# Kernel optimization log

Measured on AMD Instinct MI355X. Metric: run time of the kernel, lower is better.

The kernel has to match this reference:

```python
import jax, jax.numpy as jnp
import numpy as np

N = 50000
HEADS = 8
NEG_SLOPE = 0.2


def gat_layer(x, W, a_src, a_dst, b, src, dst, heads, n):
    # x: [N, Fin], W: [Fin, heads*C], a_src/a_dst: [heads, C], b: [heads*C]
    C = W.shape[1] // heads
    h = (x @ W).reshape(n, heads, C)                      # [N, H, C]
    al_s = jnp.einsum('nhc,hc->nh', h, a_src)             # [N, H]
    al_d = jnp.einsum('nhc,hc->nh', h, a_dst)             # [N, H]
    e = al_s[src] + al_d[dst]                             # [E, H]
    e = jnp.where(e > 0, e, NEG_SLOPE * e)                # LeakyReLU(0.2)
    # segment softmax over incoming edges of each destination node
    emax = jax.ops.segment_max(e, dst, num_segments=n)
    ex = jnp.exp(e - emax[dst])
    denom = jax.ops.segment_sum(ex, dst, num_segments=n)
    alpha = ex / denom[dst]                               # [E, H]
    out = jax.ops.segment_sum(h[src] * alpha[:, :, None], dst, num_segments=n)
    return out.reshape(n, heads * C) + b


def setup_inputs() -> dict:
    key = jax.random.key(0)
    ks = jax.random.split(key, 32)
    d_in, d_h, d_out = 128, 128, 128
    C = d_h // HEADS
    E = 800000
    x = jax.random.normal(ks[0], (N, d_in), dtype=jnp.float32)
    edge_index = jax.random.randint(ks[1], (2, E), 0, N, dtype=jnp.int64)
    edge_attr = jax.random.normal(ks[2], (E, 16), dtype=jnp.float32)
    s = lambda fan: 1.0 / np.sqrt(fan)
    inp = {'x': x, 'edge_index': edge_index, 'edge_attr': edge_attr}
    ki = 3
    for i in range(1, 5):
        fin = d_in if i == 1 else d_h
        inp[f'W{i}'] = jax.random.normal(ks[ki], (fin, d_h), jnp.float32) * s(fin); ki += 1
        inp[f'a_src{i}'] = jax.random.normal(ks[ki], (HEADS, C), jnp.float32) * s(C); ki += 1
        inp[f'a_dst{i}'] = jax.random.normal(ks[ki], (HEADS, C), jnp.float32) * s(C); ki += 1
        inp[f'b{i}'] = jnp.zeros((d_h,), jnp.float32)
    # conv5: heads=1, out=hidden
    inp['W5'] = jax.random.normal(ks[ki], (d_h, d_h), jnp.float32) * s(d_h); ki += 1
    inp['a_src5'] = jax.random.normal(ks[ki], (1, d_h), jnp.float32) * s(d_h); ki += 1
    inp['a_dst5'] = jax.random.normal(ks[ki], (1, d_h), jnp.float32) * s(d_h); ki += 1
    inp['b5'] = jnp.zeros((d_h,), jnp.float32)
    inp['W_lin'] = jax.random.normal(ks[ki], (d_h, d_out), jnp.float32) * s(d_h); ki += 1
    inp['b_lin'] = jnp.zeros((d_out,), jnp.float32)
    return inp


def reference(x, edge_index, edge_attr,
              W1, a_src1, a_dst1, b1,
              W2, a_src2, a_dst2, b2,
              W3, a_src3, a_dst3, b3,
              W4, a_src4, a_dst4, b4,
              W5, a_src5, a_dst5, b5,
              W_lin, b_lin):
    n = x.shape[0]
    # PyG GATConv adds self loops by default
    ar = jnp.arange(n, dtype=edge_index.dtype)
    src = jnp.concatenate([edge_index[0], ar])
    dst = jnp.concatenate([edge_index[1], ar])
    h = jax.nn.relu(gat_layer(x, W1, a_src1, a_dst1, b1, src, dst, HEADS, n))
    h = jax.nn.relu(gat_layer(h, W2, a_src2, a_dst2, b2, src, dst, HEADS, n))
    h = jax.nn.relu(gat_layer(h, W3, a_src3, a_dst3, b3, src, dst, HEADS, n))
    h = jax.nn.relu(gat_layer(h, W4, a_src4, a_dst4, b4, src, dst, HEADS, n))
    h = jax.nn.relu(gat_layer(h, W5, a_src5, a_dst5, b5, src, dst, 1, n))
    return jax.nn.relu(h @ W_lin + b_lin)
```

## Files before the change

### kernel.cpp

```cpp
#include <hip/hip_runtime.h>


__global__ __launch_bounds__(256) void k_deg_init(int* deg, int n) {
  int i = blockIdx.x * 256 + threadIdx.x;
  if (i < n) deg[i] = 1;
}

__global__ __launch_bounds__(256) void k_count(const int* __restrict__ ei, int E, int* deg) {
  int i = blockIdx.x * 256 + threadIdx.x;
  if (i < E) atomicAdd(&deg[ei[E + i]], 1);
}

__device__ __forceinline__ int block_excl_scan(int v, int* tot) {
  __shared__ int wsum[4];
  int lane = threadIdx.x & 63, w = threadIdx.x >> 6;
  int x = v;
  #pragma unroll
  for (int off = 1; off < 64; off <<= 1) {
    int y = __shfl_up(x, off);
    if (lane >= off) x += y;
  }
  if (lane == 63) wsum[w] = x;
  __syncthreads();
  int wbase = 0;
  #pragma unroll
  for (int i = 0; i < 4; i++) wbase += (i < w) ? wsum[i] : 0;
  if (tot) *tot = wsum[0] + wsum[1] + wsum[2] + wsum[3];
  return wbase + x - v;
}

__global__ __launch_bounds__(256) void k_bsum(const int* __restrict__ deg, int* __restrict__ bsum, int n) {
  int i = blockIdx.x * 256 + threadIdx.x;
  int v = (i < n) ? deg[i] : 0;
  int tot;
  block_excl_scan(v, &tot);
  if (threadIdx.x == 0) bsum[blockIdx.x] = tot;
}

__global__ __launch_bounds__(256) void k_bscan(const int* __restrict__ bsum, int* __restrict__ boff, int nb) {
  int t = threadIdx.x;
  int v = (t < nb) ? bsum[t] : 0;
  int ex = block_excl_scan(v, nullptr);
  if (t < nb) boff[t] = ex;
}

__global__ __launch_bounds__(256) void k_rowptr(const int* __restrict__ deg,
                                                const int* __restrict__ boff,
                                                int* __restrict__ row_ptr,
                                                int* __restrict__ cursor, int n) {
  int i = blockIdx.x * 256 + threadIdx.x;
  int v = (i < n) ? deg[i] : 0;
  int ex = block_excl_scan(v, nullptr) + boff[blockIdx.x];
  if (i < n) { row_ptr[i] = ex; cursor[i] = ex; }
  if (i == n - 1) row_ptr[n] = ex + v;
}

__global__ __launch_bounds__(256) void k_fill(const int* __restrict__ ei, int E, int n,
                                              int* cursor, int* __restrict__ srcs) {
  int i = blockIdx.x * 256 + threadIdx.x;
  if (i >= E + n) return;
  int s, d;
  if (i < E) { s = ei[i]; d = ei[E + i]; }
  else       { s = i - E; d = s; }
  int slot = atomicAdd(&cursor[d], 1);
  srcs[slot] = s;
}

__global__ __launch_bounds__(256) void k_gemm(const float* __restrict__ A,
                                              const float* __restrict__ W,
                                              const float* __restrict__ bias,
                                              float* __restrict__ C, int M, int relu) {
  __shared__ float As[32][65];
  __shared__ float Bs[32][128];
  int tid = threadIdx.x;
  int row0 = blockIdx.x * 64;
  int tx = tid & 15;
  int ty = tid >> 4;
  float acc[4][8] = {};
  for (int kt = 0; kt < 128; kt += 32) {
    #pragma unroll
    for (int i = 0; i < 2; i++) {
      int idx = tid + i * 256;
      int r = idx >> 3;
      int k4 = (idx & 7) << 2;
      float4 v = make_float4(0.f, 0.f, 0.f, 0.f);
      int gr = row0 + r;
      if (gr < M) v = *(const float4*)(A + (size_t)gr * 128 + kt + k4);
      As[k4 + 0][r] = v.x; As[k4 + 1][r] = v.y; As[k4 + 2][r] = v.z; As[k4 + 3][r] = v.w;
    }
    #pragma unroll
    for (int i = 0; i < 4; i++) {
      int idx = tid + i * 256;
      int k = idx >> 5;
      int n4 = (idx & 31) << 2;
      *(float4*)(&Bs[k][n4]) = *(const float4*)(W + (size_t)(kt + k) * 128 + n4);
    }
    __syncthreads();
    #pragma unroll
    for (int k = 0; k < 32; k++) {
      float a0 = As[k][ty * 4 + 0], a1 = As[k][ty * 4 + 1];
      float a2 = As[k][ty * 4 + 2], a3 = As[k][ty * 4 + 3];
      float b[8];
      *(float4*)&b[0] = *(const float4*)&Bs[k][tx * 8];
      *(float4*)&b[4] = *(const float4*)&Bs[k][tx * 8 + 4];
      #pragma unroll
      for (int j = 0; j < 8; j++) {
        acc[0][j] += a0 * b[j];
        acc[1][j] += a1 * b[j];
        acc[2][j] += a2 * b[j];
        acc[3][j] += a3 * b[j];
      }
    }
    __syncthreads();
  }
  #pragma unroll
  for (int i = 0; i < 4; i++) {
    int r = row0 + ty * 4 + i;
    if (r >= M) continue;
    #pragma unroll
    for (int j4 = 0; j4 < 8; j4 += 4) {
      int c = tx * 8 + j4;
      float4 v;
      v.x = acc[i][j4 + 0]; v.y = acc[i][j4 + 1];
      v.z = acc[i][j4 + 2]; v.w = acc[i][j4 + 3];
      if (bias) { v.x += bias[c]; v.y += bias[c + 1]; v.z += bias[c + 2]; v.w += bias[c + 3]; }
      if (relu) {
        v.x = fmaxf(v.x, 0.f); v.y = fmaxf(v.y, 0.f);
        v.z = fmaxf(v.z, 0.f); v.w = fmaxf(v.w, 0.f);
      }
      *(float4*)(C + (size_t)r * 128 + c) = v;
    }
  }
}

__global__ __launch_bounds__(256) void k_al8(const float* __restrict__ h,
                                             const float* __restrict__ a_s,
                                             const float* __restrict__ a_d,
                                             float* __restrict__ als, float* __restrict__ ald, int n) {
  int g = blockIdx.x * 256 + threadIdx.x;
  if (g >= n * 8) return;
  int hd = g & 7;
  const float4* hp = (const float4*)(h + (size_t)g * 16);
  const float4* ap = (const float4*)(a_s + hd * 16);
  const float4* dp = (const float4*)(a_d + hd * 16);
  float ss = 0.f, sd = 0.f;
  #pragma unroll
  for (int i = 0; i < 4; i++) {
    float4 hv = hp[i], av = ap[i], dv = dp[i];
    ss += hv.x * av.x + hv.y * av.y + hv.z * av.z + hv.w * av.w;
    sd += hv.x * dv.x + hv.y * dv.y + hv.z * dv.z + hv.w * dv.w;
  }
  als[g] = ss; ald[g] = sd;
}

__global__ __launch_bounds__(256) void k_al1(const float* __restrict__ h,
                                             const float* __restrict__ a_s,
                                             const float* __restrict__ a_d,
                                             float* __restrict__ als, float* __restrict__ ald, int n) {
  int g = blockIdx.x * 256 + threadIdx.x;
  int v = g >> 4, q = g & 15;
  bool act = (v < n);
  float ss = 0.f, sd = 0.f;
  if (act) {
    float4 hv = *(const float4*)(h + (size_t)v * 128 + q * 4);
    float4 av = *(const float4*)(a_s + q * 4);
    float4 dv = *(const float4*)(a_d + q * 4);
    ss = hv.x * av.x + hv.y * av.y + hv.z * av.z + hv.w * av.w;
    sd = hv.x * dv.x + hv.y * dv.y + hv.z * dv.z + hv.w * dv.w;
  }
  #pragma unroll
  for (int off = 1; off < 16; off <<= 1) { ss += __shfl_xor(ss, off); sd += __shfl_xor(sd, off); }
  if (act && q == 0) { als[v] = ss; ald[v] = sd; }
}

template <int H>
__global__ __launch_bounds__(256) void k_agg(const int* __restrict__ row_ptr,
                                             const int* __restrict__ srcs,
                                             const float* __restrict__ als,
                                             const float* __restrict__ ald,
                                             const float* __restrict__ h,
                                             const float* __restrict__ bias,
                                             float* __restrict__ out, int n) {
  const int EPP = 64 / H;
  int lane = threadIdx.x & 63;
  int wv = threadIdx.x >> 6;
  int v = blockIdx.x * 4 + wv;
  bool active = (v < n);
  int s0 = 0, s1 = 0;
  int eo = lane / H;
  int hd = lane % H;
  float ed = 0.f;
  if (active) { s0 = row_ptr[v]; s1 = row_ptr[v + 1]; ed = ald[v * H + hd]; }
  float m = -1e30f, d = 0.f;
  for (int j = s0 + eo; j < s1; j += EPP) {
    int sv = srcs[j];
    float e = als[sv * H + hd] + ed;
    e = (e > 0.f) ? e : 0.2f * e;
    float nm = fmaxf(m, e);
    d = d * __expf(m - nm) + __expf(e - nm);
    m = nm;
  }
  #pragma unroll
  for (int off = H; off < 64; off <<= 1) {
    float om = __shfl_xor(m, off);
    float od = __shfl_xor(d, off);
    float nm = fmaxf(m, om);
    d = d * __expf(m - nm) + od * __expf(om - nm);
    m = nm;
  }
  int slot = lane >> 5;
  int l5 = lane & 31;
  int c0 = l5 * 4;
  int hd3 = (H == 1) ? 0 : (c0 / (128 / H));
  float m3 = __shfl(m, hd3);
  float inv = 1.f / __shfl(d, hd3);
  float ed3 = __shfl(ed, hd3);
  float ax = 0.f, ay = 0.f, az = 0.f, aw = 0.f;
  #pragma unroll 2
  for (int j = s0 + slot; j < s1; j += 2) {
    int sv = srcs[j];
    float e = als[sv * H + hd3] + ed3;
    e = (e > 0.f) ? e : 0.2f * e;
    float al = __expf(e - m3) * inv;
    float4 hv = *(const float4*)(h + (size_t)sv * 128 + c0);
    ax += al * hv.x; ay += al * hv.y; az += al * hv.z; aw += al * hv.w;
  }
  ax += __shfl_xor(ax, 32);
  ay += __shfl_xor(ay, 32);
  az += __shfl_xor(az, 32);
  aw += __shfl_xor(aw, 32);
  if (active && slot == 0) {
    float4 o;
    o.x = fmaxf(ax + bias[c0 + 0], 0.f);
    o.y = fmaxf(ay + bias[c0 + 1], 0.f);
    o.z = fmaxf(az + bias[c0 + 2], 0.f);
    o.w = fmaxf(aw + bias[c0 + 3], 0.f);
    *(float4*)(out + (size_t)v * 128 + c0) = o;
  }
}

extern "C" void kernel_launch(void* const* d_in, const int* in_sizes, int n_in,
                              void* d_out, int out_size, void* d_ws, size_t ws_size,
                              hipStream_t stream) {
  const float* x  = (const float*)d_in[0];
  const int*   ei = (const int*)d_in[1];
  const int N  = in_sizes[0] / 128;
  const int E  = in_sizes[1] / 2;
  const int ET = E + N;
  const int NB = (N + 255) / 256;

  const float *Wl[5], *as[5], *ad[5], *bl[5];
  for (int l = 0; l < 5; l++) {
    Wl[l] = (const float*)d_in[3 + 4 * l];
    as[l] = (const float*)d_in[4 + 4 * l];
    ad[l] = (const float*)d_in[5 + 4 * l];
    bl[l] = (const float*)d_in[6 + 4 * l];
  }
  const float* W_lin = (const float*)d_in[23];
  const float* b_lin = (const float*)d_in[24];

  char* p = (char*)d_ws;
  auto alloc = [&](size_t bytes) { void* r = (void*)p; p += (bytes + 255) & ~size_t(255); return r; };
  float* h    = (float*)alloc((size_t)N * 128 * 4);
  float* xA   = (float*)alloc((size_t)N * 128 * 4);
  float* xB   = (float*)alloc((size_t)N * 128 * 4);
  float* als  = (float*)alloc((size_t)N * 8 * 4);
  float* ald  = (float*)alloc((size_t)N * 8 * 4);
  int* row_ptr = (int*)alloc((size_t)(N + 1) * 4);
  int* cursor  = (int*)alloc((size_t)N * 4);
  int* deg     = (int*)alloc((size_t)N * 4);
  int* srcs    = (int*)alloc((size_t)ET * 4);
  int* bsum    = (int*)alloc((size_t)NB * 4);
  int* boff    = (int*)alloc((size_t)NB * 4);
  (void)ws_size; (void)n_in; (void)out_size;

  dim3 b256(256);
  k_deg_init<<<NB, b256, 0, stream>>>(deg, N);
  k_count<<<(E + 255) / 256, b256, 0, stream>>>(ei, E, deg);
  k_bsum<<<NB, b256, 0, stream>>>(deg, bsum, N);
  k_bscan<<<1, b256, 0, stream>>>(bsum, boff, NB);
  k_rowptr<<<NB, b256, 0, stream>>>(deg, boff, row_ptr, cursor, N);
  k_fill<<<(ET + 255) / 256, b256, 0, stream>>>(ei, E, N, cursor, srcs);

  int gemm_grid = (N + 63) / 64;
  const float* xin = x;
  float* bufs[2] = { xA, xB };
  for (int l = 0; l < 5; l++) {
    float* xout = bufs[l & 1];
    k_gemm<<<gemm_grid, b256, 0, stream>>>(xin, Wl[l], nullptr, h, N, 0);
    if (l < 4) {
      k_al8<<<(N * 8 + 255) / 256, b256, 0, stream>>>(h, as[l], ad[l], als, ald, N);
      k_agg<8><<<(N + 3) / 4, b256, 0, stream>>>(row_ptr, srcs, als, ald, h, bl[l], xout, N);
    } else {
      k_al1<<<(N * 16 + 255) / 256, b256, 0, stream>>>(h, as[l], ad[l], als, ald, N);
      k_agg<1><<<(N + 3) / 4, b256, 0, stream>>>(row_ptr, srcs, als, ald, h, bl[l], xout, N);
    }
    xin = xout;
  }
  k_gemm<<<gemm_grid, b256, 0, stream>>>(xin, W_lin, b_lin, (float*)d_out, N, 1);
}
```

Before: 797.7 us.

## Replace FP32 SIMT GEMM with split-bf16 MFMA GEMM and bf16 hi/lo activations

Rewrites the dense node-feature GEMMs to use bf16 MFMA instructions. Each operand is split into hi and lo bf16 parts and three MFMAs per tile approximate FP32 accuracy. The weight matrix is converted and transposed into swizzled LDS once per block. Aggregation kernels now write activations directly as hi/lo bf16 pairs, and a conversion kernel prepares the input x. The goal is to cut GEMM compute time. The costs are extra conversion work, a 64KB LDS footprint per block that limits occupancy, and small precision loss from dropping the lo*lo term.

```diff
diff --git a/kernel.cpp b/kernel.cpp
--- a/kernel.cpp
+++ b/kernel.cpp
@@ -1,5 +1,16 @@
 #include <hip/hip_runtime.h>
 
+
+typedef short short8 __attribute__((ext_vector_type(8)));
+typedef float floatx4 __attribute__((ext_vector_type(4)));
+
+__device__ __forceinline__ unsigned short f2bf(float f) {
+  unsigned u = __float_as_uint(f);
+  return (unsigned short)((u + 0x7FFF + ((u >> 16) & 1)) >> 16);
+}
+__device__ __forceinline__ float bf2f(unsigned short h) {
+  return __uint_as_float(((unsigned)h) << 16);
+}
 
 __global__ __launch_bounds__(256) void k_deg_init(int* deg, int n) {
   int i = blockIdx.x * 256 + threadIdx.x;
@@ -66,69 +77,93 @@
   srcs[slot] = s;
 }
 
-__global__ __launch_bounds__(256) void k_gemm(const float* __restrict__ A,
-                                              const float* __restrict__ W,
-                                              const float* __restrict__ bias,
-                                              float* __restrict__ C, int M, int relu) {
-  __shared__ float As[32][65];
-  __shared__ float Bs[32][128];
+__global__ __launch_bounds__(256) void k_cvt(const float* __restrict__ x,
+                                             unsigned short* __restrict__ hi,
+                                             unsigned short* __restrict__ lo, int n4) {
+  int i = blockIdx.x * 256 + threadIdx.x;
+  if (i >= n4) return;
+  float4 v = ((const float4*)x)[i];
+  ushort4 h, l;
+  h.x = f2bf(v.x); l.x = f2bf(v.x - bf2f(h.x));
+  h.y = f2bf(v.y); l.y = f2bf(v.y - bf2f(h.y));
+  h.z = f2bf(v.z); l.z = f2bf(v.z - bf2f(h.z));
+  h.w = f2bf(v.w); l.w = f2bf(v.w - bf2f(h.w));
+  ((ushort4*)hi)[i] = h;
+  ((ushort4*)lo)[i] = l;
+}
+
+__global__ __launch_bounds__(256) void k_gemm_bf(const unsigned short* __restrict__ Ahi,
+                                                 const unsigned short* __restrict__ Alo,
+                                                 const float* __restrict__ W,
+                                                 const float* __restrict__ bias,
+                                                 float* __restrict__ C, int M, int relu) {
+  __shared__ unsigned short WtHi[128 * 128];
+  __shared__ unsigned short WtLo[128 * 128];
   int tid = threadIdx.x;
-  int row0 = blockIdx.x * 64;
-  int tx = tid & 15;
-  int ty = tid >> 4;
-  float acc[4][8] = {};
-  for (int kt = 0; kt < 128; kt += 32) {
+  #pragma unroll
+  for (int r = 0; r < 16; r++) {
+    int idx = r * 1024 + tid * 4;
+    int k = idx >> 7, n = idx & 127;
+    float4 w4 = *(const float4*)(W + idx);
+    float wf[4] = {w4.x, w4.y, w4.z, w4.w};
     #pragma unroll
-    for (int i = 0; i < 2; i++) {
-      int idx = tid + i * 256;
-      int r = idx >> 3;
-      int k4 = (idx & 7) << 2;
-      float4 v = make_float4(0.f, 0.f, 0.f, 0.f);
-      int gr = row0 + r;
-      if (gr < M) v = *(const float4*)(A + (size_t)gr * 128 + kt + k4);
-      As[k4 + 0][r] = v.x; As[k4 + 1][r] = v.y; As[k4 + 2][r] = v.z; As[k4 + 3][r] = v.w;
+    for (int e = 0; e < 4; e++) {
+      int row = n + e;
+      unsigned short hh = f2bf(wf[e]);
+      unsigned short ll = f2bf(wf[e] - bf2f(hh));
+      int di = row * 128 + (k ^ ((row & 7) << 3));
+      WtHi[di] = hh; WtLo[di] = ll;
     }
+  }
+  __syncthreads();
+
+  int lane = tid & 63;
+  int wv = tid >> 6;
+  int m0 = blockIdx.x * 64 + wv * 16;
+  int lr = lane & 15;
+  int kb = lane >> 4;
+  int arow = m0 + lr; if (arow >= M) arow = M - 1;
+  const size_t abase = (size_t)arow * 128;
+
+  short8 ahi[4], alo[4];
+  #pragma unroll
+  for (int j = 0; j < 4; j++) {
+    int k0 = j * 32 + kb * 8;
+    ahi[j] = *(const short8*)(Ahi + abase + k0);
+    alo[j] = *(const short8*)(Alo + abase + k0);
+  }
+
+  floatx4 acc[8];
+  #pragma unroll
+  for (int nt = 0; nt < 8; nt++) acc[nt] = (floatx4){0.f, 0.f, 0.f, 0.f};
+
+  #pragma unroll
+  for (int j = 0; j < 4; j++) {
     #pragma unroll
-    for (int i = 0; i < 4; i++) {
-      int idx = tid + i * 256;
-      int k = idx >> 5;
-      int n4 = (idx & 31) << 2;
-      *(float4*)(&Bs[k][n4]) = *(const float4*)(W + (size_t)(kt + k) * 128 + n4);
+    for (int nt = 0; nt < 8; nt++) {
+      int n = nt * 16 + lr;
+      int k0 = j * 32 + kb * 8;
+      int di = n * 128 + (k0 ^ ((n & 7) << 3));
+      short8 bhi = *(const short8*)(WtHi + di);
+      short8 blo = *(const short8*)(WtLo + di);
+      acc[nt] = __builtin_amdgcn_mfma_f32_16x16x32_bf16(ahi[j], bhi, acc[nt], 0, 0, 0);
+      acc[nt] = __builtin_amdgcn_mfma_f32_16x16x32_bf16(ahi[j], blo, acc[nt], 0, 0, 0);
+      acc[nt] = __builtin_amdgcn_mfma_f32_16x16x32_bf16(alo[j], bhi, acc[nt], 0, 0, 0);
     }
-    __syncthreads();
+  }
+
+  #pragma unroll
+  for (int nt = 0; nt < 8; nt++) {
+    int col = nt * 16 + lr;
     #pragma unroll
-    for (int k = 0; k < 32; k++) {
-      float a0 = As[k][ty * 4 + 0], a1 = As[k][ty * 4 + 1];
-      float a2 = As[k][ty * 4 + 2], a3 = As[k][ty * 4 + 3];
-      float b[8];
-      *(float4*)&b[0] = *(const float4*)&Bs[k][tx * 8];
-      *(float4*)&b[4] = *(const float4*)&Bs[k][tx * 8 + 4];
-      #pragma unroll
-      for (int j = 0; j < 8; j++) {
-        acc[0][j] += a0 * b[j];
-        acc[1][j] += a1 * b[j];
-        acc[2][j] += a2 * b[j];
-        acc[3][j] += a3 * b[j];
+    for (int r = 0; r < 4; r++) {
+      int row = m0 + kb * 4 + r;
+      if (row < M) {
+        float v = acc[nt][r];
+        if (bias) v += bias[col];
+        if (relu) v = fmaxf(v, 0.f);
+        C[(size_t)row * 128 + col] = v;
       }
-    }
-    __syncthreads();
-  }
-  #pragma unroll
-  for (int i = 0; i < 4; i++) {
-    int r = row0 + ty * 4 + i;
-    if (r >= M) continue;
-    #pragma unroll
-    for (int j4 = 0; j4 < 8; j4 += 4) {
-      int c = tx * 8 + j4;
-      float4 v;
-      v.x = acc[i][j4 + 0]; v.y = acc[i][j4 + 1];
-      v.z = acc[i][j4 + 2]; v.w = acc[i][j4 + 3];
-      if (bias) { v.x += bias[c]; v.y += bias[c + 1]; v.z += bias[c + 2]; v.w += bias[c + 3]; }
-      if (relu) {
-        v.x = fmaxf(v.x, 0.f); v.y = fmaxf(v.y, 0.f);
-        v.z = fmaxf(v.z, 0.f); v.w = fmaxf(v.w, 0.f);
-      }
-      *(float4*)(C + (size_t)r * 128 + c) = v;
     }
   }
 }
@@ -180,7 +215,8 @@
                                              const float* __restrict__ ald,
                                              const float* __restrict__ h,
                                              const float* __restrict__ bias,
-                                             float* __restrict__ out, int n) {
+                                             unsigned short* __restrict__ outHi,
+                                             unsigned short* __restrict__ outLo, int n) {
   const int EPP = 64 / H;
   int lane = threadIdx.x & 63;
   int wv = threadIdx.x >> 6;
@@ -230,12 +266,18 @@
   az += __shfl_xor(az, 32);
   aw += __shfl_xor(aw, 32);
   if (active && slot == 0) {
-    float4 o;
-    o.x = fmaxf(ax + bias[c0 + 0], 0.f);
-    o.y = fmaxf(ay + bias[c0 + 1], 0.f);
-    o.z = fmaxf(az + bias[c0 + 2], 0.f);
-    o.w = fmaxf(aw + bias[c0 + 3], 0.f);
-    *(float4*)(out + (size_t)v * 128 + c0) = o;
+    float o[4];
+    o[0] = fmaxf(ax + bias[c0 + 0], 0.f);
+    o[1] = fmaxf(ay + bias[c0 + 1], 0.f);
+    o[2] = fmaxf(az + bias[c0 + 2], 0.f);
+    o[3] = fmaxf(aw + bias[c0 + 3], 0.f);
+    ushort4 h4, l4;
+    h4.x = f2bf(o[0]); l4.x = f2bf(o[0] - bf2f(h4.x));
+    h4.y = f2bf(o[1]); l4.y = f2bf(o[1] - bf2f(h4.y));
+    h4.z = f2bf(o[2]); l4.z = f2bf(o[2] - bf2f(h4.z));
+    h4.w = f2bf(o[3]); l4.w = f2bf(o[3] - bf2f(h4.w));
+    *(ushort4*)(outHi + (size_t)v * 128 + c0) = h4;
+    *(ushort4*)(outLo + (size_t)v * 128 + c0) = l4;
   }
 }
 
@@ -262,8 +304,10 @@
   char* p = (char*)d_ws;
   auto alloc = [&](size_t bytes) { void* r = (void*)p; p += (bytes + 255) & ~size_t(255); return r; };
   float* h    = (float*)alloc((size_t)N * 128 * 4);
-  float* xA   = (float*)alloc((size_t)N * 128 * 4);
-  float* xB   = (float*)alloc((size_t)N * 128 * 4);
+  unsigned short* pAhi = (unsigned short*)alloc((size_t)N * 128 * 2);
+  unsigned short* pAlo = (unsigned short*)alloc((size_t)N * 128 * 2);
+  unsigned short* pBhi = (unsigned short*)alloc((size_t)N * 128 * 2);
+  unsigned short* pBlo = (unsigned short*)alloc((size_t)N * 128 * 2);
   float* als  = (float*)alloc((size_t)N * 8 * 4);
   float* ald  = (float*)alloc((size_t)N * 8 * 4);
   int* row_ptr = (int*)alloc((size_t)(N + 1) * 4);
@@ -282,20 +326,23 @@
   k_rowptr<<<NB, b256, 0, stream>>>(deg, boff, row_ptr, cursor, N);
   k_fill<<<(ET + 255) / 256, b256, 0, stream>>>(ei, E, N, cursor, srcs);
 
+  int n4 = N * 128 / 4;
+  k_cvt<<<(n4 + 255) / 256, b256, 0, stream>>>(x, pAhi, pAlo, n4);
+
   int gemm_grid = (N + 63) / 64;
-  const float* xin = x;
-  float* bufs[2] = { xA, xB };
+  unsigned short *inHi = pAhi, *inLo = pAlo, *outHi = pBhi, *outLo = pBlo;
   for (int l = 0; l < 5; l++) {
-    float* xout = bufs[l & 1];
-    k_gemm<<<gemm_grid, b256, 0, stream>>>(xin, Wl[l], nullptr, h, N, 0);
+    k_gemm_bf<<<gemm_grid, b256, 0, stream>>>(inHi, inLo, Wl[l], nullptr, h, N, 0);
     if (l < 4) {
       k_al8<<<(N * 8 + 255) / 256, b256, 0, stream>>>(h, as[l], ad[l], als, ald, N);
-      k_agg<8><<<(N + 3) / 4, b256, 0, stream>>>(row_ptr, srcs, als, ald, h, bl[l], xout, N);
+      k_agg<8><<<(N + 3) / 4, b256, 0, stream>>>(row_ptr, srcs, als, ald, h, bl[l], outHi, outLo, N);
     } else {
       k_al1<<<(N * 16 + 255) / 256, b256, 0, stream>>>(h, as[l], ad[l], als, ald, N);
-      k_agg<1><<<(N + 3) / 4, b256, 0, stream>>>(row_ptr, srcs, als, ald, h, bl[l], xout, N);
+      k_agg<1><<<(N + 3) / 4, b256, 0, stream>>>(row_ptr, srcs, als, ald, h, bl[l], outHi, outLo, N);
     }
-    xin = xout;
-  }
-  k_gemm<<<gemm_grid, b256, 0, stream>>>(xin, W_lin, b_lin, (float*)d_out, N, 1);
-}
+    unsigned short* t;
+    t = inHi; inHi = outHi; outHi = t;
+    t = inLo; inLo = outLo; outLo = t;
+  }
+  k_gemm_bf<<<gemm_grid, b256, 0, stream>>>(inHi, inLo, W_lin, b_lin, (float*)d_out, N, 1);
+}
```

After: 866.1 us. 8.6% more time.
